# Performance work log

Hardware: AMD Instinct MI355X
Metric: run time of the kernel (lower is better)

## Reference

```python
import jax, jax.numpy as jnp
import numpy as np
from jax import lax

N_SAMPLES = 2 ** 15          # 32768
N_FRAMES = 128
N_HARMONICS = 8
FILT_SIZE = 64
N_EVENTS = 8
N_SCALE = 128                # len(MusicalScale()) assumed = 128 (MIDI notes)
NYQ = 11025.0                # SR22050 nyquist
MIN_F0 = 40.0 / NYQ
MAX_F0 = 3000.0 / NYQ
F0_SPAN = MAX_F0 - MIN_F0
MIN_RES = 0.9
RES_SPAN = 1.0 - MIN_RES
PI = float(np.pi)

# packed layout slices (order of param_sizes dict)
SL_F0 = slice(0, 128)
SL_FINE = slice(128, 256)
SL_AMP = slice(256, 384)
SL_HAMP = slice(384, 392)
SL_HDEC = slice(392, 400)
SL_FENV = slice(400, 464)


def lin_interp(x, out_size):
    """F.interpolate(mode='linear', align_corners=False) along last axis."""
    n = x.shape[-1]
    pos = (jnp.arange(out_size, dtype=x.dtype) + 0.5) * (n / out_size) - 0.5
    pos = jnp.clip(pos, 0.0, n - 1)
    lo = jnp.floor(pos).astype(jnp.int32)
    hi = jnp.minimum(lo + 1, n - 1)
    w = pos - lo.astype(x.dtype)
    return x[..., lo] * (1.0 - w) + x[..., hi] * w


def setup_inputs() -> dict:
    key = jax.random.key(0)
    k1, k2 = jax.random.split(key)
    B = 32 * N_EVENTS  # 256 event rows
    packed = jax.random.normal(k1, (B, 464), dtype=jnp.float32)
    # musical scale: MIDI-note center frequencies normalized by nyquist
    midi = np.arange(N_SCALE)
    freqs = 440.0 * 2.0 ** ((midi - 69) / 12.0) / NYQ
    frequencies = jnp.asarray(freqs, dtype=jnp.float32)
    noise = jax.random.uniform(k2, (B, 1, N_SAMPLES), dtype=jnp.float32)  # mapped to (-1,1) in reference
    return {"packed": packed, "frequencies": frequencies, "noise": noise}


def reference(packed, frequencies, noise):
    B = packed.shape[0]
    p = jax.nn.sigmoid(packed)  # Model applies activation(p) before SynthParams

    # f0: softmax over discrete scale bins, weighted sum of normalized freqs
    f0w = jax.nn.softmax(p[:, SL_F0], axis=-1)             # [B, 128]
    f0 = (f0w @ frequencies)[:, None, None]                # [B,1,1]
    f0 = jnp.broadcast_to(f0, (B, 1, N_FRAMES))            # repeat over frames
    f0 = f0 * NYQ
    f0 = MIN_F0 + f0 * F0_SPAN                             # [B,1,128]
    # NOTE: source computes `f0 + f0 + f0_fine` and discards it -> f0_fine unused

    harmonic_factors = jnp.arange(1, N_HARMONICS + 1, dtype=p.dtype)
    osc = f0 * harmonic_factors[None, :, None]             # [B,8,128]
    radians = osc / NYQ * PI
    radians = lin_interp(radians, N_SAMPLES)               # [B,8,32768]
    osc_bank = jnp.sin(jnp.cumsum(radians, axis=-1))

    harm_decay = MIN_RES + p[:, SL_HDEC] * RES_SPAN        # [B,8]
    harm_amp = p[:, SL_HAMP]                               # [B,8]
    amp = p[:, SL_AMP][:, None, :] * 2.0 - 1.0             # [B,1,128]
    amp_full = lin_interp(amp, N_SAMPLES)                  # [B,1,32768]

    noise_filter = p[:, SL_FENV][:, None, :]               # [B,1,64]
    noise_filter = lin_interp(noise_filter, N_SAMPLES // 2)
    noise_filter = jnp.pad(noise_filter, ((0, 0), (0, 0), (0, 1)))  # [B,1,16385]

    noise_u = noise * 2.0 - 1.0                            # uniform(-1,1)
    noise_spec = jnp.fft.rfft(noise_u, axis=-1, norm='ortho')
    filt = jnp.fft.irfft(noise_spec * noise_filter, n=N_SAMPLES, axis=-1, norm='ortho')
    filt = filt * jnp.clip(amp_full, 0.0, 1.0)             # [B,1,32768]

    # leaky-accumulator recurrence over frames
    def step(cur, a_i):  # cur [B,8], a_i [B]
        cur = jnp.clip(cur + a_i[:, None] * harm_amp, 0.0, 1.0)
        out = cur
        cur = cur * harm_decay
        return cur, out

    amp_t = amp[:, 0, :].T                                 # [128, B]
    _, outs = lax.scan(step, jnp.zeros((B, N_HARMONICS), dtype=p.dtype), amp_t)
    x = jnp.transpose(outs, (1, 2, 0))                     # [B,8,128]
    x = jnp.where(x >= PI, 0.0, x)
    x = lin_interp(x, N_SAMPLES)                           # [B,8,32768]
    x = x * osc_bank
    x = filt + x
    x = x.reshape(-1, N_EVENTS, N_HARMONICS, N_SAMPLES)
    x = jnp.sum(x, axis=(1, 2))[:, None, :]                # [batch,1,32768]
    return x
```

## Files before the change

kernel.cpp:

```cpp
#include <hip/hip_runtime.h>
#include <math.h>

#ifndef M_PI
#define M_PI 3.14159265358979323846
#endif

#define NSAMP 32768
#define MHALF 16384
#define TWO_PI_F 6.2831853071795864f
#define PSTRIDE 1089

typedef float v2 __attribute__((ext_vector_type(2)));

__device__ __forceinline__ double dsig(double x) { return 1.0 / (1.0 + exp(-x)); }

__device__ __forceinline__ v2 cmul(v2 a, v2 b) {
    return a.xx * b + (v2){-a.y, a.y} * b.yx;
}

template<int INV>
__device__ __forceinline__ void fft4(v2& x0, v2& x1, v2& x2, v2& x3) {
    v2 s02 = x0 + x2;
    v2 d02 = x0 - x2;
    v2 s13 = x1 + x3;
    v2 d13 = x1 - x3;
    v2 j13 = INV ? (v2){-d13.y, d13.x} : (v2){d13.y, -d13.x};
    x0 = s02 + s13;
    x2 = s02 - s13;
    x1 = d02 + j13;
    x3 = d02 - j13;
}

#define V16(v, c) v[((((c) & 3) << 2) | ((c) >> 2))]

template<int INV>
__device__ __forceinline__ void fft16(v2 v[16]) {
    const float s = INV ? 1.0f : -1.0f;
#pragma unroll
    for (int b = 0; b < 4; b++) fft4<INV>(v[b], v[4 + b], v[8 + b], v[12 + b]);
    v[5]  = cmul(v[5],  (v2){0.9238795325f,  s * 0.3826834324f});
    v[9]  = cmul(v[9],  (v2){0.7071067812f,  s * 0.7071067812f});
    v[13] = cmul(v[13], (v2){0.3826834324f,  s * 0.9238795325f});
    v[6]  = cmul(v[6],  (v2){0.7071067812f,  s * 0.7071067812f});
    v[10] = cmul(v[10], (v2){0.0f,           s * 1.0f});
    v[14] = cmul(v[14], (v2){-0.7071067812f, s * 0.7071067812f});
    v[7]  = cmul(v[7],  (v2){0.3826834324f,  s * 0.9238795325f});
    v[11] = cmul(v[11], (v2){-0.7071067812f, s * 0.7071067812f});
    v[15] = cmul(v[15], (v2){-0.9238795325f, s * -0.3826834324f});
#pragma unroll
    for (int p = 0; p < 4; p++) fft4<INV>(v[4 * p], v[4 * p + 1], v[4 * p + 2], v[4 * p + 3]);
}

__device__ __forceinline__ int zaddr(int k) {
    int p = k & 15, k2 = k >> 4;
    int s = 256 * (k2 & 3) + 16 * ((k2 >> 2) & 15) + (k2 >> 6);
    return p * PSTRIDE + s + (s >> 4);
}

__device__ __forceinline__ void plane_fwd(v2* __restrict__ Zp, int l) {
    {
        float sn, cs;
        __sincosf(TWO_PI_F * (float)l * (1.f / 1024.f), &sn, &cs);
        v2 w1 = (v2){cs, -sn};
        const v2 jstep = (v2){0.9238795325f, -0.3826834324f};
#pragma unroll
        for (int j = 0; j < 4; j++) {
            const int r = 64 * j + l;
            v2 u0 = Zp[r], u1 = Zp[256 + r], u2 = Zp[512 + r], u3 = Zp[768 + r];
            fft4<0>(u0, u1, u2, u3);
            v2 w2 = cmul(w1, w1);
            v2 w3 = cmul(w2, w1);
            Zp[r] = u0;
            Zp[256 + r] = cmul(u1, w1);
            Zp[512 + r] = cmul(u2, w2);
            Zp[768 + r] = cmul(u3, w3);
            w1 = cmul(w1, jstep);
        }
    }
    {
        const int k4 = l >> 4, c = l & 15;
        const int nbase = 256 * k4 + c;
        float sn, cs;
        __sincosf(TWO_PI_F * (float)c * (1.f / 256.f), &sn, &cs);
        const v2 wc = (v2){cs, -sn};
        v2 v[16];
#pragma unroll
        for (int b = 0; b < 16; b++) v[b] = Zp[nbase + 16 * b];
        fft16<0>(v);
        const int pbase = 272 * k4 + c;
        Zp[pbase] = V16(v, 0);
        v2 w = wc;
#pragma unroll
        for (int kb = 1; kb < 16; kb++) {
            Zp[pbase + 17 * kb] = cmul(V16(v, kb), w);
            w = cmul(w, wc);
        }
    }
    {
        const int pbase = 272 * (l >> 4) + 17 * (l & 15);
        v2 v[16];
#pragma unroll
        for (int c = 0; c < 16; c++) v[c] = Zp[pbase + c];
        fft16<0>(v);
#pragma unroll
        for (int kc = 0; kc < 16; kc++) Zp[pbase + kc] = V16(v, kc);
    }
}

__device__ __forceinline__ void plane_inv(v2* __restrict__ Zp, int l) {
    {
        const int kb = l & 15;
        const int pbase = 272 * (l >> 4) + 17 * kb;
        float sn, cs;
        __sincosf(TWO_PI_F * (float)kb * (1.f / 256.f), &sn, &cs);
        const v2 wkb = (v2){cs, sn};
        v2 v[16];
#pragma unroll
        for (int kc = 0; kc < 16; kc++) v[kc] = Zp[pbase + kc];
        fft16<1>(v);
        Zp[pbase] = V16(v, 0);
        v2 w = wkb;
#pragma unroll
        for (int nc = 1; nc < 16; nc++) {
            Zp[pbase + nc] = cmul(V16(v, nc), w);
            w = cmul(w, wkb);
        }
    }
    {
        const int k4 = l >> 4, nc = l & 15;
        const int pbase = 272 * k4 + nc;
        float sni, csi;
        __sincosf(TWO_PI_F * (float)(nc * k4) * (1.f / 1024.f), &sni, &csi);
        v2 t = (v2){csi, sni};
        float sns, css;
        __sincosf(TWO_PI_F * (float)k4 * (1.f / 64.f), &sns, &css);
        const v2 st = (v2){css, sns};
        v2 v[16];
#pragma unroll
        for (int kb = 0; kb < 16; kb++) v[kb] = Zp[pbase + 17 * kb];
        fft16<1>(v);
#pragma unroll
        for (int nb = 0; nb < 16; nb++) {
            Zp[pbase + 17 * nb] = cmul(V16(v, nb), t);
            t = cmul(t, st);
        }
    }
#pragma unroll
    for (int j = 0; j < 4; j++) {
        const int r = 64 * j + l;
        const int rp = r + (r >> 4);
        v2 u0 = Zp[rp], u1 = Zp[272 + rp], u2 = Zp[544 + rp], u3 = Zp[816 + rp];
        fft4<1>(u0, u1, u2, u3);
        Zp[rp] = u0; Zp[272 + rp] = u1; Zp[544 + rp] = u2; Zp[816 + rp] = u3;
    }
}

__device__ __forceinline__ float hinterp64(const float* f, int j) {
    float pos = ((float)j + 0.5f) * (1.0f / 256.0f) - 0.5f;
    pos = fminf(fmaxf(pos, 0.0f), 63.0f);
    int lo = (int)pos;
    int hi = min(lo + 1, 63);
    float w = pos - (float)lo;
    return f[lo] * (1.0f - w) + f[hi] * w;
}

template<int J>
__device__ __forceinline__ void synth_chunk(
    int tid, const float* __restrict__ env_s,
    const unsigned long long* __restrict__ step_s, float* __restrict__ po)
{
    const int s0 = (tid << 2) + (J << 12);

    float c0v[4], c1v[4], c2v[4];
    float pos0 = ((float)s0 + 0.5f) * (1.0f / 256.0f) - 0.5f;
    pos0 = fminf(fmaxf(pos0, 0.0f), 127.0f);
    const int lo0 = (int)pos0;
#pragma unroll
    for (int k = 0; k < 4; k++) {
        float pos = ((float)(s0 + k) + 0.5f) * (1.0f / 256.0f) - 0.5f;
        pos = fminf(fmaxf(pos, 0.0f), 127.0f);
        int lo = (int)pos;
        float w = pos - (float)lo;
        if (lo == lo0) { c0v[k] = 1.0f - w; c1v[k] = w;        c2v[k] = 0.0f; }
        else           { c0v[k] = 0.0f;     c1v[k] = 1.0f - w; c2v[k] = w;    }
    }
    const int i1 = min(lo0 + 1, 127);
    float pos3 = ((float)(s0 + 3) + 0.5f) * (1.0f / 256.0f) - 0.5f;
    pos3 = fminf(fmaxf(pos3, 0.0f), 127.0f);
    const int i2 = min((int)pos3 + 1, 127);

    float a0 = 0.f, a1 = 0.f, a2 = 0.f, a3 = 0.f;
    const unsigned long long n0 = (unsigned long long)(unsigned)(s0 + 1);

#pragma unroll
    for (int h = 0; h < 8; h++) {
        const unsigned long long st = step_s[h];
        const unsigned long long pp = st * n0;
        const float stf = (float)(unsigned)(st >> 32) * 0x1p-32f;
        float fr = (float)(unsigned)(pp >> 32) * 0x1p-32f;
        const float* er = env_s + (h << 7);
        const float v0 = er[lo0], v1 = er[i1], ve2 = er[i2];

        float ev, sn;

        sn = __builtin_amdgcn_sinf(fr);
        ev = fmaf(v0, c0v[0], fmaf(v1, c1v[0], ve2 * c2v[0]));
        a0 = fmaf(ev, sn, a0);
        fr = __builtin_amdgcn_fractf(fr + stf);

        sn = __builtin_amdgcn_sinf(fr);
        ev = fmaf(v0, c0v[1], fmaf(v1, c1v[1], ve2 * c2v[1]));
        a1 = fmaf(ev, sn, a1);
        fr = __builtin_amdgcn_fractf(fr + stf);

        sn = __builtin_amdgcn_sinf(fr);
        ev = fmaf(v0, c0v[2], fmaf(v1, c1v[2], ve2 * c2v[2]));
        a2 = fmaf(ev, sn, a2);
        fr = __builtin_amdgcn_fractf(fr + stf);

        sn = __builtin_amdgcn_sinf(fr);
        ev = fmaf(v0, c0v[3], fmaf(v1, c1v[3], ve2 * c2v[3]));
        a3 = fmaf(ev, sn, a3);
    }

    float4 r;
    r.x = a0; r.y = a1; r.z = a2; r.w = a3;
    *(float4*)(po + s0) = r;
}

__global__ __launch_bounds__(1024, 4) void fused_kernel(
    const float* __restrict__ packed, const float* __restrict__ freqs,
    const float* __restrict__ noise, float* __restrict__ part)
{
    __shared__ v2 Z[16 * PSTRIDE];
    __shared__ float fenv_s[64];
    __shared__ float amp_s[128];
    __shared__ double ampd_s[128];
    __shared__ float env_s[8 * 128];
    __shared__ unsigned long long step_s[8];

    const int bb = blockIdx.x;
    const int tid = threadIdx.x;
    const int wv = tid >> 6, l = tid & 63;

    float* po_sine = part + ((size_t)(256 + bb) << 15);

    if (tid < 64) {
        const float* pk = packed + bb * 464;
        double e0 = exp(dsig((double)pk[tid]));
        double e1 = exp(dsig((double)pk[tid + 64]));
        double num = e0 * (double)freqs[tid] + e1 * (double)freqs[tid + 64];
        double den = e0 + e1;
#pragma unroll
        for (int off = 32; off > 0; off >>= 1) {
            num += __shfl_down(num, off);
            den += __shfl_down(den, off);
        }
        num = __shfl(num, 0);
        den = __shfl(den, 0);

        double a0 = dsig((double)pk[256 + tid]) * 2.0 - 1.0;
        double a1 = dsig((double)pk[256 + 64 + tid]) * 2.0 - 1.0;
        ampd_s[tid] = a0; ampd_s[tid + 64] = a1;
        amp_s[tid] = (float)a0; amp_s[tid + 64] = (float)a1;
        fenv_s[tid] = (float)dsig((double)pk[400 + tid]);

        if (tid < 8) {
            const double NYQ = 11025.0;
            const double MIN_F0 = 40.0 / NYQ;
            const double MAX_F0 = 3000.0 / NYQ;
            const double F0_SPAN = MAX_F0 - MIN_F0;
            double f0 = num / den;
            double F = f0 * NYQ;
            double G = MIN_F0 + F * F0_SPAN;
            double oscf = G * (double)(tid + 1);
            double r = oscf / NYQ * M_PI;
            double rv = r / (2.0 * M_PI);
            rv -= floor(rv);
            step_s[tid] = (unsigned long long)(rv * 18446744073709551616.0);

            double ha = dsig((double)pk[384 + tid]);
            double hd = 0.9 + dsig((double)pk[392 + tid]) * (1.0 - 0.9);
            double cur = 0.0;
            float* eo = env_s + (tid << 7);
            for (int fr = 0; fr < 128; fr++) {
                cur = cur + ampd_s[fr] * ha;
                cur = fmin(fmax(cur, 0.0), 1.0);
                eo[fr] = (float)cur;
                cur *= hd;
            }
        }
    }

    const v2* nz = (const v2*)(noise + (size_t)bb * NSAMP);

    {
        v2 v[16];
#pragma unroll
        for (int a = 0; a < 16; a++) {
            v2 t = nz[a * 1024 + tid];
            v[a] = t * 2.f - 1.f;
        }
        fft16<0>(v);
        float sn, cs;
        __sincosf(TWO_PI_F * (float)tid * (1.f / 16384.f), &sn, &cs);
        const v2 ws = (v2){cs, -sn};
        Z[tid] = V16(v, 0);
        v2 w = ws;
#pragma unroll
        for (int k1 = 1; k1 < 16; k1++) {
            Z[k1 * PSTRIDE + tid] = cmul(V16(v, k1), w);
            w = cmul(w, ws);
        }
    }
    __syncthreads();

    synth_chunk<0>(tid, env_s, step_s, po_sine);
    synth_chunk<1>(tid, env_s, step_s, po_sine);

    plane_fwd(Z + wv * PSTRIDE, l);

    synth_chunk<2>(tid, env_s, step_s, po_sine);
    synth_chunk<3>(tid, env_s, step_s, po_sine);
    __syncthreads();

    const float invM = 1.0f / (float)MHALF;
    {
        float sn0, cs0;
        __sincosf((float)M_PI * (float)tid * (1.f / 16384.f), &sn0, &cs0);
        v2 t = (v2){cs0, sn0};
        const v2 tstep = (v2){0.98078528040323f, 0.19509032201613f};
        for (int k = tid; k <= 8192; k += 1024) {
            if (k == 0) {
                int i0 = zaddr(0);
                v2 Z0 = Z[i0];
                float Y0 = (Z0.x + Z0.y) * hinterp64(fenv_s, 0);
                float vv = Y0 * 0.5f * invM;
                Z[i0] = (v2){vv, vv};
            } else if (k == 8192) {
                int i8 = zaddr(8192);
                float s = hinterp64(fenv_s, 8192) * invM;
                Z[i8] = Z[i8] * s;
            } else {
                int ik = zaddr(k), imk = zaddr(16384 - k);
                v2 Zk = Z[ik], Zm = Z[imk];
                float Ex = 0.5f * (Zk.x + Zm.x);
                float Ey = 0.5f * (Zk.y - Zm.y);
                float Ox = 0.5f * (Zk.y + Zm.y);
                float Oy = -0.5f * (Zk.x - Zm.x);
                float cs = t.x, sn = t.y;
                float Xkx = Ex + cs * Ox + sn * Oy;
                float Xky = Ey + cs * Oy - sn * Ox;
                float Xmx = Ex - cs * Ox - sn * Oy;
                float Xmy = -Ey + cs * Oy - sn * Ox;
                float Hk = hinterp64(fenv_s, k);
                float Hm = hinterp64(fenv_s, 16384 - k);
                float Ykx = Xkx * Hk, Yky = Xky * Hk;
                float Ymx = Xmx * Hm, Ymy = Xmy * Hm;
                float Er = 0.5f * (Ykx + Ymx);
                float Ei = 0.5f * (Yky - Ymy);
                float Pr = 0.5f * (Ykx - Ymx);
                float Pi = 0.5f * (Yky + Ymy);
                float Oyx = Pr * cs - Pi * sn;
                float Oyy = Pr * sn + Pi * cs;
                Z[ik]  = (v2){(Er - Oyy) * invM, (Ei + Oyx) * invM};
                Z[imk] = (v2){(Er + Oyy) * invM, (-Ei + Oyx) * invM};
            }
            t = cmul(t, tstep);
        }
    }

    synth_chunk<4>(tid, env_s, step_s, po_sine);
    synth_chunk<5>(tid, env_s, step_s, po_sine);
    __syncthreads();

    plane_inv(Z + wv * PSTRIDE, l);

    synth_chunk<6>(tid, env_s, step_s, po_sine);
    synth_chunk<7>(tid, env_s, step_s, po_sine);
    __syncthreads();

    {
        const int tp = tid + (tid >> 4);
        v2 v[16];
#pragma unroll
        for (int k1 = 0; k1 < 16; k1++) v[k1] = Z[k1 * PSTRIDE + tp];
        float sn, cs;
        __sincosf(TWO_PI_F * (float)tid * (1.f / 16384.f), &sn, &cs);
        const v2 wg = (v2){cs, sn};
        v2 w = wg;
#pragma unroll
        for (int k1 = 1; k1 < 16; k1++) {
            v[k1] = cmul(v[k1], w);
            w = cmul(w, wg);
        }
        fft16<1>(v);

        v2* fo = (v2*)(part + ((size_t)bb << 15));
#pragma unroll
        for (int m = 0; m < 16; m++) {
            v2 y = V16(v, m);
            int A = m * 1024 + tid;
            int s0 = 2 * A;
            float p0 = ((float)s0 + 0.5f) * (1.0f / 256.0f) - 0.5f;
            float p1 = p0 + (1.0f / 256.0f);
            p0 = fminf(fmaxf(p0, 0.0f), 127.0f);
            p1 = fminf(fmaxf(p1, 0.0f), 127.0f);
            int l0 = (int)p0, l1 = (int)p1;
            int h0 = min(l0 + 1, 127), h1 = min(l1 + 1, 127);
            float w0a = p0 - (float)l0, w1a = p1 - (float)l1;
            float a0 = amp_s[l0] * (1.0f - w0a) + amp_s[h0] * w0a;
            float a1 = amp_s[l1] * (1.0f - w1a) + amp_s[h1] * w1a;
            a0 = fminf(fmaxf(a0, 0.0f), 1.0f);
            a1 = fminf(fmaxf(a1, 0.0f), 1.0f);
            fo[A] = (v2){8.0f * y.x * a0, 8.0f * y.y * a1};
        }
    }
}

__global__ __launch_bounds__(256) void reduce_kernel(
    const float* __restrict__ part, float* __restrict__ out)
{
    const int t = blockIdx.x * 256 + threadIdx.x;
    const int g = t >> 13;
    const int s = (t & 8191) << 2;

    float4 a = make_float4(0.f, 0.f, 0.f, 0.f);
#pragma unroll
    for (int e = 0; e < 8; e++) {
        const float4 f = *(const float4*)(part + ((size_t)(g * 8 + e) << 15) + s);
        const float4 sn = *(const float4*)(part + ((size_t)(256 + g * 8 + e) << 15) + s);
        a.x += f.x + sn.x; a.y += f.y + sn.y;
        a.z += f.z + sn.z; a.w += f.w + sn.w;
    }
    *(float4*)(out + ((size_t)g << 15) + s) = a;
}

extern "C" void kernel_launch(void* const* d_in, const int* in_sizes, int n_in,
                              void* d_out, int out_size, void* d_ws, size_t ws_size,
                              hipStream_t stream)
{
    (void)in_sizes; (void)n_in; (void)out_size; (void)ws_size;
    const float* packed = (const float*)d_in[0];
    const float* freqs  = (const float*)d_in[1];
    const float* noise  = (const float*)d_in[2];
    float* out = (float*)d_out;
    float* part = (float*)d_ws;

    hipLaunchKernelGGL(fused_kernel, dim3(256), dim3(1024), 0, stream,
                       packed, freqs, noise, part);
    hipLaunchKernelGGL(reduce_kernel, dim3(1024), dim3(256), 0, stream,
                       part, out);
}
```

Before: 139.5 us.

## Use Chebyshev sine recurrence for harmonics, float envelope, remap blocks for locality

The sine-bank loop now takes one sin and one cos of the fundamental phase per sample and builds the eight harmonics with the Chebyshev recurrence sin((h+1)x)=2cos(x)sin(hx)-sin((h-1)x). This replaces eight transcendental calls per sample with FMAs. The envelope recurrence and amp storage move from double to float, and the double shared array is removed. Block-to-event and reduce block-to-chunk mappings are permuted, apparently for cache or XCD locality, and launch bounds become an explicit waves-per-EU attribute. The recurrence and float accumulation can drift from the exact per-harmonic phases.

```diff
diff --git a/kernel.cpp b/kernel.cpp
--- a/kernel.cpp
+++ b/kernel.cpp
@@ -189,57 +189,54 @@
     pos3 = fminf(fmaxf(pos3, 0.0f), 127.0f);
     const int i2 = min((int)pos3 + 1, 127);
 
-    float a0 = 0.f, a1 = 0.f, a2 = 0.f, a3 = 0.f;
-    const unsigned long long n0 = (unsigned long long)(unsigned)(s0 + 1);
-
+    float v0a[8], v1a[8], v2a[8];
 #pragma unroll
     for (int h = 0; h < 8; h++) {
-        const unsigned long long st = step_s[h];
-        const unsigned long long pp = st * n0;
-        const float stf = (float)(unsigned)(st >> 32) * 0x1p-32f;
-        float fr = (float)(unsigned)(pp >> 32) * 0x1p-32f;
         const float* er = env_s + (h << 7);
-        const float v0 = er[lo0], v1 = er[i1], ve2 = er[i2];
-
-        float ev, sn;
-
-        sn = __builtin_amdgcn_sinf(fr);
-        ev = fmaf(v0, c0v[0], fmaf(v1, c1v[0], ve2 * c2v[0]));
-        a0 = fmaf(ev, sn, a0);
-        fr = __builtin_amdgcn_fractf(fr + stf);
-
-        sn = __builtin_amdgcn_sinf(fr);
-        ev = fmaf(v0, c0v[1], fmaf(v1, c1v[1], ve2 * c2v[1]));
-        a1 = fmaf(ev, sn, a1);
-        fr = __builtin_amdgcn_fractf(fr + stf);
-
-        sn = __builtin_amdgcn_sinf(fr);
-        ev = fmaf(v0, c0v[2], fmaf(v1, c1v[2], ve2 * c2v[2]));
-        a2 = fmaf(ev, sn, a2);
-        fr = __builtin_amdgcn_fractf(fr + stf);
-
-        sn = __builtin_amdgcn_sinf(fr);
-        ev = fmaf(v0, c0v[3], fmaf(v1, c1v[3], ve2 * c2v[3]));
-        a3 = fmaf(ev, sn, a3);
-    }
-
-    float4 r;
-    r.x = a0; r.y = a1; r.z = a2; r.w = a3;
-    *(float4*)(po + s0) = r;
-}
-
-__global__ __launch_bounds__(1024, 4) void fused_kernel(
+        v0a[h] = er[lo0]; v1a[h] = er[i1]; v2a[h] = er[i2];
+    }
+
+    const unsigned long long st1 = step_s[0];
+    const float stf1 = (float)(unsigned)(st1 >> 32) * 0x1p-32f;
+    const unsigned long long pp = st1 * (unsigned long long)(unsigned)(s0 + 1);
+    float fr = (float)(unsigned)(pp >> 32) * 0x1p-32f;
+
+    float out[4];
+#pragma unroll
+    for (int k = 0; k < 4; k++) {
+        const float sn = __builtin_amdgcn_sinf(fr);
+        const float cs = __builtin_amdgcn_cosf(fr);
+        const float c2 = cs + cs;
+        float s_prev = 0.0f, s_cur = sn;
+        float a = 0.0f;
+#pragma unroll
+        for (int h = 0; h < 8; h++) {
+            const float ev = fmaf(v0a[h], c0v[k], fmaf(v1a[h], c1v[k], v2a[h] * c2v[k]));
+            a = fmaf(ev, s_cur, a);
+            const float s_next = fmaf(c2, s_cur, -s_prev);
+            s_prev = s_cur; s_cur = s_next;
+        }
+        out[k] = a;
+        fr = __builtin_amdgcn_fractf(fr + stf1);
+    }
+    *(float4*)(po + s0) = make_float4(out[0], out[1], out[2], out[3]);
+}
+
+__global__ __launch_bounds__(1024)
+__attribute__((amdgpu_waves_per_eu(4, 4)))
+void fused_kernel(
     const float* __restrict__ packed, const float* __restrict__ freqs,
     const float* __restrict__ noise, float* __restrict__ part)
 {
     __shared__ v2 Z[16 * PSTRIDE];
     __shared__ float fenv_s[64];
     __shared__ float amp_s[128];
-    __shared__ double ampd_s[128];
     __shared__ float env_s[8 * 128];
     __shared__ unsigned long long step_s[8];
 
-    const int bb = blockIdx.x;
+    const int bid = blockIdx.x;
+    const int g = (bid & 7) + 8 * ((bid >> 3) & 3);
+    const int bb = g * 8 + (bid >> 5);
     const int tid = threadIdx.x;
     const int wv = tid >> 6, l = tid & 63;
 
@@ -259,10 +256,9 @@
         num = __shfl(num, 0);
         den = __shfl(den, 0);
 
-        double a0 = dsig((double)pk[256 + tid]) * 2.0 - 1.0;
-        double a1 = dsig((double)pk[256 + 64 + tid]) * 2.0 - 1.0;
-        ampd_s[tid] = a0; ampd_s[tid + 64] = a1;
-        amp_s[tid] = (float)a0; amp_s[tid + 64] = (float)a1;
+        float a0 = (float)(dsig((double)pk[256 + tid]) * 2.0 - 1.0);
+        float a1 = (float)(dsig((double)pk[256 + 64 + tid]) * 2.0 - 1.0);
+        amp_s[tid] = a0; amp_s[tid + 64] = a1;
         fenv_s[tid] = (float)dsig((double)pk[400 + tid]);
 
         if (tid < 8) {
@@ -279,14 +275,14 @@
             rv -= floor(rv);
             step_s[tid] = (unsigned long long)(rv * 18446744073709551616.0);
 
-            double ha = dsig((double)pk[384 + tid]);
-            double hd = 0.9 + dsig((double)pk[392 + tid]) * (1.0 - 0.9);
-            double cur = 0.0;
+            float ha = (float)dsig((double)pk[384 + tid]);
+            float hd = 0.9f + (float)dsig((double)pk[392 + tid]) * 0.1f;
+            float cur = 0.0f;
             float* eo = env_s + (tid << 7);
             for (int fr = 0; fr < 128; fr++) {
-                cur = cur + ampd_s[fr] * ha;
-                cur = fmin(fmax(cur, 0.0), 1.0);
-                eo[fr] = (float)cur;
+                cur = fmaf(amp_s[fr], ha, cur);
+                cur = fminf(fmaxf(cur, 0.0f), 1.0f);
+                eo[fr] = cur;
                 cur *= hd;
             }
         }
@@ -421,14 +417,15 @@
 __global__ __launch_bounds__(256) void reduce_kernel(
     const float* __restrict__ part, float* __restrict__ out)
 {
-    const int t = blockIdx.x * 256 + threadIdx.x;
-    const int g = t >> 13;
-    const int s = (t & 8191) << 2;
+    const int b = blockIdx.x;
+    const int g = (b & 7) + 8 * ((b >> 3) & 3);
+    const int chunk = b >> 5;
+    const int s = (chunk << 10) + ((int)threadIdx.x << 2);
 
     float4 a = make_float4(0.f, 0.f, 0.f, 0.f);
 #pragma unroll
     for (int e = 0; e < 8; e++) {
-        const float4 f = *(const float4*)(part + ((size_t)(g * 8 + e) << 15) + s);
+        const float4 f  = *(const float4*)(part + ((size_t)(g * 8 + e) << 15) + s);
         const float4 sn = *(const float4*)(part + ((size_t)(256 + g * 8 + e) << 15) + s);
         a.x += f.x + sn.x; a.y += f.y + sn.y;
         a.z += f.z + sn.z; a.w += f.w + sn.w;
```

New measurement: 120.2 us (median of 2 runs). 13.8% less time.
